# Optimization experiments

Measured on AMD Instinct MI355X. Metric: run time of the kernel, lower is better.

The kernel has to match this reference:

```python
import jax, jax.numpy as jnp
import numpy as np

B, H, W, C = 8, 64, 64, 512
CK, CV = C // 8, C // 2  # 64, 256


def maxpool2x2(x):
    # x: [B, H, W, C] -> [B, H//2, W//2, C], 2x2 max pool, stride 2 (keras MaxPooling2D default)
    b, h, w, c = x.shape
    return x.reshape(b, h // 2, 2, w // 2, 2, c).max(axis=(2, 4))


def setup_inputs() -> dict:
    key = jax.random.key(0)
    ks = jax.random.split(key, 6)
    wscale = 0.02
    return {
        "x": jax.random.normal(ks[0], (B, H, W, C), dtype=jnp.float32),
        "w_theta": jax.random.normal(ks[1], (C, CK), dtype=jnp.float32) * wscale,
        "w_phi": jax.random.normal(ks[2], (C, CK), dtype=jnp.float32) * wscale,
        "w_g": jax.random.normal(ks[3], (C, CV), dtype=jnp.float32) * wscale,
        "w_o": jax.random.normal(ks[4], (CV, C), dtype=jnp.float32) * wscale,
        "gamma": jax.random.normal(ks[5], (1,), dtype=jnp.float32),
    }


def reference(x, w_theta, w_phi, w_g, w_o, gamma):
    b, h, w, c = x.shape
    hw = h * w
    # theta: 1x1 conv -> [B, HW, C//8]
    theta = jnp.einsum('bhwc,ck->bhwk', x, w_theta).reshape(b, hw, -1)
    # phi: 1x1 conv + 2x2 maxpool -> [B, HW//4, C//8]
    phi = maxpool2x2(jnp.einsum('bhwc,ck->bhwk', x, w_phi)).reshape(b, hw // 4, -1)
    # attention: [B, HW, HW//4], softmax over last axis
    attn = jax.nn.softmax(jnp.einsum('bqk,bpk->bqp', theta, phi), axis=-1)
    # g: 1x1 conv + 2x2 maxpool -> [B, HW//4, C//2]
    g = maxpool2x2(jnp.einsum('bhwc,cv->bhwv', x, w_g)).reshape(b, hw // 4, -1)
    # attn_g: [B, HW, C//2] -> [B, H, W, C//2] -> 1x1 conv -> [B, H, W, C]
    attn_g = jnp.einsum('bqp,bpv->bqv', attn, g).reshape(b, h, w, -1)
    attn_g = jnp.einsum('bhwv,vc->bhwc', attn_g, w_o)
    return x + gamma * attn_g
```

## Files before the change

kernel.cpp:

```cpp
#include <hip/hip_runtime.h>
#include <hip/hip_bf16.h>
#include <cstddef>
#include <cstdint>


typedef __attribute__((ext_vector_type(8))) short short8;
typedef __attribute__((ext_vector_type(4))) float float4v;

namespace {
constexpr int kB = 8, kC = 512, kCK = 64, kCV = 256, kHW = 4096, kP = 1024;
constexpr int kNP = 384;
}

__device__ __forceinline__ void gll16(const void* g, void* l) {
  __builtin_amdgcn_global_load_lds((uint32_t __attribute__((address_space(1)))*)g,
                                   (uint32_t __attribute__((address_space(3)))*)l,
                                   16, 0, 0);
}
__device__ __forceinline__ float4v mfma16(short8 a, short8 b, float4v c) {
  return __builtin_amdgcn_mfma_f32_16x16x32_bf16(a, b, c, 0, 0, 0);
}
__device__ __forceinline__ const short8* fragp(const char* tile, int row, int oct) {
  return (const short8*)(tile + row * 128 + ((oct ^ (row & 7)) * 16));
}

__global__ __launch_bounds__(256) void k_pack_w(
    const float* __restrict__ wt, const float* __restrict__ wphi,
    const float* __restrict__ wg, const float* __restrict__ wo,
    __hip_bfloat16* __restrict__ wAll, __hip_bfloat16* __restrict__ woT) {
  int idx = blockIdx.x * 256 + threadIdx.x;
  if (idx < 196608) {
    int n = idx >> 9, k = idx & 511;
    float v = (n < 64) ? wt[k * 64 + n]
            : (n < 128) ? wphi[k * 64 + (n - 64)]
                        : wg[k * 256 + (n - 128)];
    wAll[idx] = __float2bfloat16(v);
  } else {
    int t = idx - 196608;
    int n = t >> 8, k = t & 255;
    woT[t] = __float2bfloat16(wo[k * 512 + n]);
  }
}

__global__ __launch_bounds__(256) void k_proj(const float* __restrict__ x,
                                              const __hip_bfloat16* __restrict__ wAll,
                                              __hip_bfloat16* __restrict__ pgf) {
  __shared__ __align__(16) char smem[16384 + 49152];
  char* As = smem;
  char* Bs = smem + 16384;
  const int tid = threadIdx.x, wid = tid >> 6, lane = tid & 63;
  const int m = lane & 15, quad = lane >> 4;
  const int row0 = blockIdx.x * 64;
  const int wm = (wid >> 1) * 32, wn = (wid & 1) * 192;
  float4v acc[2][12] = {};
  for (int kc = 0; kc < 512; kc += 64) {
#pragma unroll
    for (int u = 0; u < 4; ++u) {
      const int r0 = (wid * 4 + u) * 4;
      const int row = r0 + (lane >> 4);
      const int sqg = (lane & 15) ^ (row & 15);
      gll16(x + (size_t)(row0 + row) * 512 + kc + sqg * 4, As + r0 * 256);
    }
#pragma unroll
    for (int u = 0; u < 12; ++u) {
      const int r0 = (wid * 12 + u) * 8;
      const int row = r0 + (lane >> 3);
      const int og = (lane & 7) ^ (row & 7);
      gll16(wAll + (size_t)row * 512 + kc + og * 8, Bs + r0 * 128);
    }
    __syncthreads();
#pragma unroll
    for (int kk = 0; kk < 64; kk += 32) {
      short8 af[2];
#pragma unroll
      for (int i = 0; i < 2; ++i) {
        const int row = wm + i * 16 + m;
        const int sq0 = (kk >> 2) + quad * 2;
        float4v lo = *(const float4v*)(As + row * 256 + ((sq0 ^ m) * 16));
        float4v hi = *(const float4v*)(As + row * 256 + (((sq0 + 1) ^ m) * 16));
        short8 a;
        a[0] = __builtin_bit_cast(short, __float2bfloat16(lo[0]));
        a[1] = __builtin_bit_cast(short, __float2bfloat16(lo[1]));
        a[2] = __builtin_bit_cast(short, __float2bfloat16(lo[2]));
        a[3] = __builtin_bit_cast(short, __float2bfloat16(lo[3]));
        a[4] = __builtin_bit_cast(short, __float2bfloat16(hi[0]));
        a[5] = __builtin_bit_cast(short, __float2bfloat16(hi[1]));
        a[6] = __builtin_bit_cast(short, __float2bfloat16(hi[2]));
        a[7] = __builtin_bit_cast(short, __float2bfloat16(hi[3]));
        af[i] = a;
      }
      const int oct = (kk >> 3) + quad;
#pragma unroll
      for (int j = 0; j < 12; ++j) {
        short8 bf = *fragp(Bs, wn + j * 16 + m, oct);
#pragma unroll
        for (int i = 0; i < 2; ++i) acc[i][j] = mfma16(af[i], bf, acc[i][j]);
      }
    }
    __syncthreads();
  }
#pragma unroll
  for (int i = 0; i < 2; ++i)
#pragma unroll
    for (int j = 0; j < 12; ++j)
#pragma unroll
      for (int r = 0; r < 4; ++r)
        pgf[(size_t)(row0 + wm + i * 16 + quad * 4 + r) * 384 + wn + j * 16 + m] =
            __float2bfloat16(acc[i][j][r]);
}

__global__ __launch_bounds__(256) void k_pool_phi(const __hip_bfloat16* __restrict__ pg,
                                                  __hip_bfloat16* __restrict__ phi_p) {
  int idx = blockIdx.x * 256 + threadIdx.x;
  int c = idx & 63;
  int p = (idx >> 6) & 1023;
  int b = idx >> 16;
  int ph = p >> 5, pw = p & 31;
  size_t base = ((size_t)b * 4096 + ph * 128 + pw * 2) * kNP + 64 + c;
  float v0 = __bfloat162float(pg[base]);
  float v1 = __bfloat162float(pg[base + kNP]);
  float v2 = __bfloat162float(pg[base + kNP * 64]);
  float v3 = __bfloat162float(pg[base + kNP * 64 + kNP]);
  phi_p[idx] = __float2bfloat16(fmaxf(fmaxf(v0, v1), fmaxf(v2, v3)));
}

__global__ __launch_bounds__(256) void k_pool_gT(const __hip_bfloat16* __restrict__ pg,
                                                 __hip_bfloat16* __restrict__ gT) {
  __shared__ __hip_bfloat16 t[64][65];
  const int p0 = blockIdx.x * 64, v0 = blockIdx.y * 64, b = blockIdx.z;
#pragma unroll
  for (int it = 0; it < 16; ++it) {
    int li = it * 256 + threadIdx.x;
    int pp = li >> 6, v = li & 63;
    int p = p0 + pp;
    int ph = p >> 5, pw = p & 31;
    size_t base = ((size_t)b * 4096 + ph * 128 + pw * 2) * kNP + 128 + v0 + v;
    float mv = fmaxf(
        fmaxf(__bfloat162float(pg[base]), __bfloat162float(pg[base + kNP])),
        fmaxf(__bfloat162float(pg[base + kNP * 64]), __bfloat162float(pg[base + kNP * 64 + kNP])));
    t[pp][v] = __float2bfloat16(mv);
  }
  __syncthreads();
#pragma unroll
  for (int it = 0; it < 16; ++it) {
    int li = it * 256 + threadIdx.x;
    int v = li >> 6, p = li & 63;
    gT[((size_t)b * 256 + v0 + v) * 1024 + p0 + p] = t[p][v];
  }
}

__global__ __launch_bounds__(1024) void k_fattn(
    const __hip_bfloat16* __restrict__ pgf,
    const __hip_bfloat16* __restrict__ phip,
    const __hip_bfloat16* __restrict__ gT,
    __hip_bfloat16* __restrict__ O) {
  __shared__ __align__(16) char smem[131072 + 2048 + 256];
  char* P = smem;
  float* pred = (float*)(smem + 131072);
  float* rowstat = (float*)(smem + 131072 + 2048);

  const int tid = threadIdx.x, wid = tid >> 6, lane = tid & 63;
  const int m = lane & 15, quad = lane >> 4;
  const int bid = blockIdx.x;
  const int b = bid & 7;
  const int q0 = (bid >> 3) * 64;
  const int qh = wid & 1;
  const int kw = wid >> 1;

  short8 aq[2][2];
  const __hip_bfloat16* qb = pgf + (size_t)(b * kHW + q0 + qh * 32) * kNP;
#pragma unroll
  for (int i = 0; i < 2; ++i)
#pragma unroll
    for (int t = 0; t < 2; ++t)
      aq[i][t] = *(const short8*)(qb + (size_t)(i * 16 + m) * kNP + t * 32 + quad * 8);

  const __hip_bfloat16* kbp = phip + ((size_t)b * kP + kw * 128) * 64;
  float4v sc[2][8] = {};
  short8 kf[2][2];
#pragma unroll
  for (int t = 0; t < 2; ++t)
    kf[0][t] = *(const short8*)(kbp + (size_t)m * 64 + t * 32 + quad * 8);
#pragma unroll
  for (int c = 0; c < 8; ++c) {
    if (c < 7) {
#pragma unroll
      for (int t = 0; t < 2; ++t)
        kf[(c + 1) & 1][t] =
            *(const short8*)(kbp + (size_t)((c + 1) * 16 + m) * 64 + t * 32 + quad * 8);
    }
#pragma unroll
    for (int t = 0; t < 2; ++t)
#pragma unroll
      for (int i = 0; i < 2; ++i) sc[i][c] = mfma16(aq[i][t], kf[c & 1][t], sc[i][c]);
  }

  float mx[2][4];
#pragma unroll
  for (int i = 0; i < 2; ++i)
#pragma unroll
    for (int r = 0; r < 4; ++r) {
      float v = sc[i][0][r];
#pragma unroll
      for (int s = 1; s < 8; ++s) v = fmaxf(v, sc[i][s][r]);
#pragma unroll
      for (int d = 1; d < 16; d <<= 1) v = fmaxf(v, __shfl_xor(v, d));
      mx[i][r] = v;
    }
  if (m == 0) {
#pragma unroll
    for (int i = 0; i < 2; ++i)
#pragma unroll
      for (int r = 0; r < 4; ++r)
        pred[(qh * 32 + i * 16 + quad * 4 + r) * 8 + kw] = mx[i][r];
  }
  __syncthreads();
  if (tid < 64) {
    float v = pred[tid * 8];
#pragma unroll
    for (int w = 1; w < 8; ++w) v = fmaxf(v, pred[tid * 8 + w]);
    rowstat[tid] = v;
  }
  __syncthreads();
  float sm[2][4];
#pragma unroll
  for (int i = 0; i < 2; ++i)
#pragma unroll
    for (int r = 0; r < 4; ++r) {
      const float rm = rowstat[qh * 32 + i * 16 + quad * 4 + r];
      float s = 0.f;
#pragma unroll
      for (int ss = 0; ss < 8; ++ss) {
        float e = __expf(sc[i][ss][r] - rm);
        sc[i][ss][r] = e;
        s += e;
      }
#pragma unroll
      for (int d = 1; d < 16; d <<= 1) s += __shfl_xor(s, d);
      sm[i][r] = s;
    }
  if (m == 0) {
#pragma unroll
    for (int i = 0; i < 2; ++i)
#pragma unroll
      for (int r = 0; r < 4; ++r)
        pred[(qh * 32 + i * 16 + quad * 4 + r) * 8 + kw] = sm[i][r];
  }
  __syncthreads();
  if (tid < 64) {
    float s = 0.f;
#pragma unroll
    for (int w = 0; w < 8; ++w) s += pred[tid * 8 + w];
    rowstat[tid] = 1.f / s;
  }
  __syncthreads();

#pragma unroll
  for (int i = 0; i < 2; ++i)
#pragma unroll
    for (int c = 0; c < 8; ++c)
#pragma unroll
      for (int r = 0; r < 4; ++r) {
        const int row = qh * 32 + i * 16 + quad * 4 + r;
        const int key = kw * 128 + c * 16 + m;
        const int oct = key >> 3;
        const int oc2 = (oct & 0x70) | ((oct & 15) ^ (row & 15));
        *(__hip_bfloat16*)(P + row * 2048 + oc2 * 16 + (key & 7) * 2) =
            __float2bfloat16(sc[i][c][r]);
      }
  __syncthreads();

  const __hip_bfloat16* gbase = gT + ((size_t)b * kCV + wid * 16 + m) * kP;
  float4v oc[4] = {};
  short8 gf[2];
  gf[0] = *(const short8*)(gbase + quad * 8);
#pragma unroll
  for (int cp = 0; cp < 32; ++cp) {
    const int cur = cp & 1;
    if (cp < 31) gf[cur ^ 1] = *(const short8*)(gbase + (cp + 1) * 32 + quad * 8);
    short8 af[4];
#pragma unroll
    for (int i = 0; i < 4; ++i) {
      const int row = i * 16 + m;
      const int oct = cp * 4 + quad;
      const int oc2 = (oct & 0x70) | ((oct & 15) ^ (row & 15));
      af[i] = *(const short8*)(P + row * 2048 + oc2 * 16);
    }
#pragma unroll
    for (int i = 0; i < 4; ++i) oc[i] = mfma16(af[i], gf[cur], oc[i]);
  }

#pragma unroll
  for (int i = 0; i < 4; ++i)
#pragma unroll
    for (int r = 0; r < 4; ++r) {
      const int row = i * 16 + quad * 4 + r;
      O[((size_t)b * kHW + q0 + row) * kCV + wid * 16 + m] =
          __float2bfloat16(oc[i][r] * rowstat[row]);
    }
}

__global__ __launch_bounds__(256) void k_out(const __hip_bfloat16* __restrict__ A,
                                             const __hip_bfloat16* __restrict__ Bw,
                                             const float* __restrict__ x,
                                             const float* __restrict__ gamma,
                                             float* __restrict__ out) {
  __shared__ __align__(16) char smem[4 * 16384];
  const int tid = threadIdx.x, wid = tid >> 6, lane = tid & 63;
  const int m = lane & 15, quad = lane >> 4;
  const int row0 = blockIdx.x * 128, col0 = blockIdx.y * 128;
  const int wm = (wid >> 1) * 64, wn = (wid & 1) * 64;
  float4v acc[4][4] = {};
  auto stage = [&](int t, int buf) {
    const int kc = t * 64;
#pragma unroll
    for (int u = 0; u < 4; ++u) {
      const int r0 = (wid * 4 + u) * 8;
      const int row = r0 + (lane >> 3);
      const int og = (lane & 7) ^ (row & 7);
      gll16(A + (size_t)(row0 + row) * 256 + kc + og * 8, smem + buf * 16384 + r0 * 128);
      gll16(Bw + (size_t)(col0 + row) * 256 + kc + og * 8,
            smem + 32768 + buf * 16384 + r0 * 128);
    }
  };
  stage(0, 0);
  __syncthreads();
#pragma unroll
  for (int t = 0; t < 4; ++t) {
    if (t < 3) stage(t + 1, (t + 1) & 1);
    const char* Ab = smem + (t & 1) * 16384;
    const char* Bb = smem + 32768 + (t & 1) * 16384;
    __builtin_amdgcn_s_setprio(1);
#pragma unroll
    for (int kk = 0; kk < 64; kk += 32) {
      const int oct = (kk >> 3) + quad;
      short8 af[4], bf[4];
#pragma unroll
      for (int i = 0; i < 4; ++i) af[i] = *fragp(Ab, wm + i * 16 + m, oct);
#pragma unroll
      for (int j = 0; j < 4; ++j) bf[j] = *fragp(Bb, wn + j * 16 + m, oct);
#pragma unroll
      for (int i = 0; i < 4; ++i)
#pragma unroll
        for (int j = 0; j < 4; ++j) acc[i][j] = mfma16(af[i], bf[j], acc[i][j]);
    }
    __builtin_amdgcn_s_setprio(0);
    __syncthreads();
  }
  const float g = gamma[0];
#pragma unroll
  for (int i = 0; i < 4; ++i)
#pragma unroll
    for (int j = 0; j < 4; ++j) {
      const int cc = col0 + wn + j * 16 + m;
      const int rb = row0 + wm + i * 16 + quad * 4;
#pragma unroll
      for (int r = 0; r < 4; ++r) {
        const size_t idx = (size_t)(rb + r) * 512 + cc;
        out[idx] = x[idx] + g * acc[i][j][r];
      }
    }
}

extern "C" void kernel_launch(void* const* d_in, const int* in_sizes, int n_in,
                              void* d_out, int out_size, void* d_ws, size_t ws_size,
                              hipStream_t stream) {
  (void)in_sizes; (void)n_in; (void)out_size; (void)ws_size;
  const float* x     = (const float*)d_in[0];
  const float* wt    = (const float*)d_in[1];
  const float* wphi  = (const float*)d_in[2];
  const float* wg    = (const float*)d_in[3];
  const float* wo    = (const float*)d_in[4];
  const float* gamma = (const float*)d_in[5];
  float* out = (float*)d_out;

  char* ws = (char*)d_ws;
  __hip_bfloat16* wAll = (__hip_bfloat16*)(ws);
  __hip_bfloat16* woT  = (__hip_bfloat16*)(ws + 393216);
  __hip_bfloat16* pgf  = (__hip_bfloat16*)(ws + 655360);
  __hip_bfloat16* phip = (__hip_bfloat16*)(ws + 25821184);
  __hip_bfloat16* gT   = (__hip_bfloat16*)(ws + 26869760);
  __hip_bfloat16* O    = (__hip_bfloat16*)(ws + 31064064);

  k_pack_w<<<1280, 256, 0, stream>>>(wt, wphi, wg, wo, wAll, woT);
  k_proj<<<512, 256, 0, stream>>>(x, wAll, pgf);
  k_pool_phi<<<2048, 256, 0, stream>>>(pgf, phip);
  k_pool_gT<<<dim3(16, 4, 8), 256, 0, stream>>>(pgf, gT);
  k_fattn<<<dim3(kHW / 64 * kB), 1024, 0, stream>>>(pgf, phip, gT, O);
  k_out<<<dim3(256, 4), 256, 0, stream>>>(O, woT, x, gamma, out);
}
```

Before: 234.9 us.

## Repartition attention waves over all query rows and split PV across key halves

Each of the 16 waves in the fused attention kernel now computes all 64 query rows against a 64-key slice, where before each wave handled 32 rows against 128 keys. This reuses the query fragments and deepens key prefetch to three buffers. The PV stage now gives each wave a 64x32 output tile over half of the keys, reusing A and G fragments more and prefetching deeper. A shared-memory reduction then combines the two key-halves. One barrier before the P write is dropped, the reduction adds LDS traffic and two barriers, and the higher register pressure is capped by a launch_bounds hint.

```diff
diff --git a/kernel.cpp b/kernel.cpp
--- a/kernel.cpp
+++ b/kernel.cpp
@@ -149,120 +149,104 @@
   }
 }
 
-__global__ __launch_bounds__(1024) void k_fattn(
+__global__ __launch_bounds__(1024, 4) void k_fattn(
     const __hip_bfloat16* __restrict__ pgf,
     const __hip_bfloat16* __restrict__ phip,
     const __hip_bfloat16* __restrict__ gT,
     __hip_bfloat16* __restrict__ O) {
-  __shared__ __align__(16) char smem[131072 + 2048 + 256];
+  __shared__ __align__(16) char smem[131072 + 4096 + 256];
   char* P = smem;
   float* pred = (float*)(smem + 131072);
-  float* rowstat = (float*)(smem + 131072 + 2048);
+  float* rowstat = (float*)(smem + 131072 + 4096);
 
   const int tid = threadIdx.x, wid = tid >> 6, lane = tid & 63;
   const int m = lane & 15, quad = lane >> 4;
   const int bid = blockIdx.x;
   const int b = bid & 7;
   const int q0 = (bid >> 3) * 64;
-  const int qh = wid & 1;
-  const int kw = wid >> 1;
-
-  short8 aq[2][2];
-  const __hip_bfloat16* qb = pgf + (size_t)(b * kHW + q0 + qh * 32) * kNP;
-#pragma unroll
-  for (int i = 0; i < 2; ++i)
+
+  short8 aq[4][2];
+  const __hip_bfloat16* qb = pgf + (size_t)(b * kHW + q0) * kNP;
+#pragma unroll
+  for (int i = 0; i < 4; ++i)
 #pragma unroll
     for (int t = 0; t < 2; ++t)
       aq[i][t] = *(const short8*)(qb + (size_t)(i * 16 + m) * kNP + t * 32 + quad * 8);
 
-  const __hip_bfloat16* kbp = phip + ((size_t)b * kP + kw * 128) * 64;
-  float4v sc[2][8] = {};
-  short8 kf[2][2];
-#pragma unroll
-  for (int t = 0; t < 2; ++t)
+  const __hip_bfloat16* kbp = phip + ((size_t)b * kP + wid * 64) * 64;
+  float4v sc[4][4] = {};
+  short8 kf[3][2];
+#pragma unroll
+  for (int t = 0; t < 2; ++t) {
     kf[0][t] = *(const short8*)(kbp + (size_t)m * 64 + t * 32 + quad * 8);
-#pragma unroll
-  for (int c = 0; c < 8; ++c) {
-    if (c < 7) {
+    kf[1][t] = *(const short8*)(kbp + (size_t)(16 + m) * 64 + t * 32 + quad * 8);
+  }
+#pragma unroll
+  for (int c = 0; c < 4; ++c) {
+    if (c < 2) {
 #pragma unroll
       for (int t = 0; t < 2; ++t)
-        kf[(c + 1) & 1][t] =
-            *(const short8*)(kbp + (size_t)((c + 1) * 16 + m) * 64 + t * 32 + quad * 8);
+        kf[(c + 2) % 3][t] =
+            *(const short8*)(kbp + (size_t)((c + 2) * 16 + m) * 64 + t * 32 + quad * 8);
     }
 #pragma unroll
     for (int t = 0; t < 2; ++t)
 #pragma unroll
-      for (int i = 0; i < 2; ++i) sc[i][c] = mfma16(aq[i][t], kf[c & 1][t], sc[i][c]);
-  }
-
-  float mx[2][4];
-#pragma unroll
-  for (int i = 0; i < 2; ++i)
+      for (int i = 0; i < 4; ++i) sc[i][c] = mfma16(aq[i][t], kf[c % 3][t], sc[i][c]);
+  }
+
+#pragma unroll
+  for (int i = 0; i < 4; ++i) {
 #pragma unroll
     for (int r = 0; r < 4; ++r) {
       float v = sc[i][0][r];
 #pragma unroll
-      for (int s = 1; s < 8; ++s) v = fmaxf(v, sc[i][s][r]);
+      for (int c = 1; c < 4; ++c) v = fmaxf(v, sc[i][c][r]);
 #pragma unroll
       for (int d = 1; d < 16; d <<= 1) v = fmaxf(v, __shfl_xor(v, d));
-      mx[i][r] = v;
-    }
-  if (m == 0) {
-#pragma unroll
-    for (int i = 0; i < 2; ++i)
-#pragma unroll
-      for (int r = 0; r < 4; ++r)
-        pred[(qh * 32 + i * 16 + quad * 4 + r) * 8 + kw] = mx[i][r];
+      if (m == 0) pred[(i * 16 + quad * 4 + r) * 16 + wid] = v;
+    }
   }
   __syncthreads();
   if (tid < 64) {
-    float v = pred[tid * 8];
-#pragma unroll
-    for (int w = 1; w < 8; ++w) v = fmaxf(v, pred[tid * 8 + w]);
+    float v = pred[tid * 16];
+#pragma unroll
+    for (int w = 1; w < 16; ++w) v = fmaxf(v, pred[tid * 16 + w]);
     rowstat[tid] = v;
   }
   __syncthreads();
-  float sm[2][4];
-#pragma unroll
-  for (int i = 0; i < 2; ++i)
+#pragma unroll
+  for (int i = 0; i < 4; ++i)
 #pragma unroll
     for (int r = 0; r < 4; ++r) {
-      const float rm = rowstat[qh * 32 + i * 16 + quad * 4 + r];
+      const float rm = rowstat[i * 16 + quad * 4 + r];
       float s = 0.f;
 #pragma unroll
-      for (int ss = 0; ss < 8; ++ss) {
-        float e = __expf(sc[i][ss][r] - rm);
-        sc[i][ss][r] = e;
+      for (int c = 0; c < 4; ++c) {
+        float e = __expf(sc[i][c][r] - rm);
+        sc[i][c][r] = e;
         s += e;
       }
 #pragma unroll
       for (int d = 1; d < 16; d <<= 1) s += __shfl_xor(s, d);
-      sm[i][r] = s;
-    }
-  if (m == 0) {
-#pragma unroll
-    for (int i = 0; i < 2; ++i)
-#pragma unroll
-      for (int r = 0; r < 4; ++r)
-        pred[(qh * 32 + i * 16 + quad * 4 + r) * 8 + kw] = sm[i][r];
-  }
+      if (m == 0) pred[(i * 16 + quad * 4 + r) * 16 + wid] = s;
+    }
   __syncthreads();
   if (tid < 64) {
     float s = 0.f;
 #pragma unroll
-    for (int w = 0; w < 8; ++w) s += pred[tid * 8 + w];
+    for (int w = 0; w < 16; ++w) s += pred[tid * 16 + w];
     rowstat[tid] = 1.f / s;
   }
-  __syncthreads();
-
-#pragma unroll
-  for (int i = 0; i < 2; ++i)
-#pragma unroll
-    for (int c = 0; c < 8; ++c)
+
+#pragma unroll
+  for (int i = 0; i < 4; ++i)
+#pragma unroll
+    for (int c = 0; c < 4; ++c)
 #pragma unroll
       for (int r = 0; r < 4; ++r) {
-        const int row = qh * 32 + i * 16 + quad * 4 + r;
-        const int key = kw * 128 + c * 16 + m;
+        const int row = i * 16 + quad * 4 + r;
+        const int key = wid * 64 + c * 16 + m;
         const int oct = key >> 3;
         const int oc2 = (oct & 0x70) | ((oct & 15) ^ (row & 15));
         *(__hip_bfloat16*)(P + row * 2048 + oc2 * 16 + (key & 7) * 2) =
@@ -270,34 +254,70 @@
       }
   __syncthreads();
 
-  const __hip_bfloat16* gbase = gT + ((size_t)b * kCV + wid * 16 + m) * kP;
-  float4v oc[4] = {};
-  short8 gf[2];
-  gf[0] = *(const short8*)(gbase + quad * 8);
-#pragma unroll
-  for (int cp = 0; cp < 32; ++cp) {
-    const int cur = cp & 1;
-    if (cp < 31) gf[cur ^ 1] = *(const short8*)(gbase + (cp + 1) * 32 + quad * 8);
-    short8 af[4];
-#pragma unroll
-    for (int i = 0; i < 4; ++i) {
-      const int row = i * 16 + m;
-      const int oct = cp * 4 + quad;
-      const int oc2 = (oct & 0x70) | ((oct & 15) ^ (row & 15));
-      af[i] = *(const short8*)(P + row * 2048 + oc2 * 16);
-    }
-#pragma unroll
-    for (int i = 0; i < 4; ++i) oc[i] = mfma16(af[i], gf[cur], oc[i]);
-  }
-
-#pragma unroll
-  for (int i = 0; i < 4; ++i)
-#pragma unroll
-    for (int r = 0; r < 4; ++r) {
-      const int row = i * 16 + quad * 4 + r;
-      O[((size_t)b * kHW + q0 + row) * kCV + wid * 16 + m] =
-          __float2bfloat16(oc[i][r] * rowstat[row]);
-    }
+  const int g = wid >> 3, w8 = wid & 7;
+  const __hip_bfloat16* gb = gT + ((size_t)b * kCV + w8 * 32) * kP + g * 512;
+  float4v oc[4][2] = {};
+  short8 gf[3][2], af[2][4];
+  auto ldG = [&](int cp, int j) {
+    return *(const short8*)(gb + (size_t)(j * 16 + m) * kP + cp * 32 + quad * 8);
+  };
+  auto ldA = [&](int cp, int i) {
+    const int row = i * 16 + m;
+    const int oct = (g * 16 + cp) * 4 + quad;
+    const int oc2 = (oct & 0x70) | ((oct & 15) ^ (row & 15));
+    return *(const short8*)(P + row * 2048 + oc2 * 16);
+  };
+#pragma unroll
+  for (int j = 0; j < 2; ++j) {
+    gf[0][j] = ldG(0, j);
+    gf[1][j] = ldG(1, j);
+  }
+#pragma unroll
+  for (int i = 0; i < 4; ++i) af[0][i] = ldA(0, i);
+#pragma unroll
+  for (int cp = 0; cp < 16; ++cp) {
+    if (cp < 15) {
+#pragma unroll
+      for (int i = 0; i < 4; ++i) af[(cp + 1) & 1][i] = ldA(cp + 1, i);
+    }
+    if (cp < 14) {
+#pragma unroll
+      for (int j = 0; j < 2; ++j) gf[(cp + 2) % 3][j] = ldG(cp + 2, j);
+    }
+#pragma unroll
+    for (int i = 0; i < 4; ++i)
+#pragma unroll
+      for (int j = 0; j < 2; ++j)
+        oc[i][j] = mfma16(af[cp & 1][i], gf[cp % 3][j], oc[i][j]);
+  }
+
+  __syncthreads();
+  float* Pf = (float*)smem;
+  if (g == 1) {
+#pragma unroll
+    for (int i = 0; i < 4; ++i)
+#pragma unroll
+      for (int j = 0; j < 2; ++j)
+#pragma unroll
+        for (int r = 0; r < 4; ++r) {
+          const int row = i * 16 + quad * 4 + r;
+          Pf[row * 260 + w8 * 32 + j * 16 + m] = oc[i][j][r];
+        }
+  }
+  __syncthreads();
+  if (g == 0) {
+#pragma unroll
+    for (int i = 0; i < 4; ++i)
+#pragma unroll
+      for (int j = 0; j < 2; ++j)
+#pragma unroll
+        for (int r = 0; r < 4; ++r) {
+          const int row = i * 16 + quad * 4 + r;
+          const int col = w8 * 32 + j * 16 + m;
+          const float s = (oc[i][j][r] + Pf[row * 260 + col]) * rowstat[row];
+          O[((size_t)b * kHW + q0 + row) * kCV + col] = __float2bfloat16(s);
+        }
+  }
 }
 
 __global__ __launch_bounds__(256) void k_out(const __hip_bfloat16* __restrict__ A,
```

New measurement: 241.4 us. 1.03x slower.

## Rewrite attention as single-wave online-softmax flash kernel with register-resident P

Applied to the files above, without the earlier changes.

Replaces the 1024-thread block attention kernel, which kept the full 64x1024 probability tile in LDS and used block-wide syncs for the softmax statistics. The new kernel runs one wave per block. Each block handles 32 queries and 128 value channels and streams keys in chunks of 64 with an online softmax. Probabilities are repacked from the QK accumulator layout into the PV input-fragment layout using cross-lane shuffles, so LDS and barriers are not needed. The cost is recomputing QK^T once per value group (twice overall), plus heavy register pressure and many uncoalesced per-lane global loads of K and G with no LDS staging.

```diff
diff --git a/kernel.cpp b/kernel.cpp
--- a/kernel.cpp
+++ b/kernel.cpp
@@ -6,6 +6,7 @@
 
 typedef __attribute__((ext_vector_type(8))) short short8;
 typedef __attribute__((ext_vector_type(4))) float float4v;
+typedef __attribute__((ext_vector_type(4))) uint32_t uint4v;
 
 namespace {
 constexpr int kB = 8, kC = 512, kCK = 64, kCV = 256, kHW = 4096, kP = 1024;
@@ -22,6 +23,17 @@
 }
 __device__ __forceinline__ const short8* fragp(const char* tile, int row, int oct) {
   return (const short8*)(tile + row * 128 + ((oct ^ (row & 7)) * 16));
+}
+__device__ __forceinline__ uint32_t packbf(float a, float b) {
+  const uint32_t lo = (uint32_t)__builtin_bit_cast(unsigned short, __float2bfloat16(a));
+  const uint32_t hi = (uint32_t)__builtin_bit_cast(unsigned short, __float2bfloat16(b));
+  return lo | (hi << 16);
+}
+__device__ __forceinline__ uint32_t sx16(uint32_t v) {
+  return (uint32_t)__shfl_xor((int)v, 16);
+}
+__device__ __forceinline__ uint32_t sx32(uint32_t v) {
+  return (uint32_t)__shfl_xor((int)v, 32);
 }
 
 __global__ __launch_bounds__(256) void k_pack_w(
@@ -149,155 +161,148 @@
   }
 }
 
-__global__ __launch_bounds__(1024) void k_fattn(
+__global__ __launch_bounds__(64, 2) void k_fattn(
     const __hip_bfloat16* __restrict__ pgf,
     const __hip_bfloat16* __restrict__ phip,
     const __hip_bfloat16* __restrict__ gT,
     __hip_bfloat16* __restrict__ O) {
-  __shared__ __align__(16) char smem[131072 + 2048 + 256];
-  char* P = smem;
-  float* pred = (float*)(smem + 131072);
-  float* rowstat = (float*)(smem + 131072 + 2048);
-
-  const int tid = threadIdx.x, wid = tid >> 6, lane = tid & 63;
+  const int lane = threadIdx.x;
   const int m = lane & 15, quad = lane >> 4;
   const int bid = blockIdx.x;
   const int b = bid & 7;
-  const int q0 = (bid >> 3) * 64;
-  const int qh = wid & 1;
-  const int kw = wid >> 1;
-
-  short8 aq[2][2];
-  const __hip_bfloat16* qb = pgf + (size_t)(b * kHW + q0 + qh * 32) * kNP;
-#pragma unroll
-  for (int i = 0; i < 2; ++i)
-#pragma unroll
-    for (int t = 0; t < 2; ++t)
-      aq[i][t] = *(const short8*)(qb + (size_t)(i * 16 + m) * kNP + t * 32 + quad * 8);
-
-  const __hip_bfloat16* kbp = phip + ((size_t)b * kP + kw * 128) * 64;
-  float4v sc[2][8] = {};
-  short8 kf[2][2];
-#pragma unroll
-  for (int t = 0; t < 2; ++t)
-    kf[0][t] = *(const short8*)(kbp + (size_t)m * 64 + t * 32 + quad * 8);
-#pragma unroll
-  for (int c = 0; c < 8; ++c) {
-    if (c < 7) {
-#pragma unroll
-      for (int t = 0; t < 2; ++t)
-        kf[(c + 1) & 1][t] =
-            *(const short8*)(kbp + (size_t)((c + 1) * 16 + m) * 64 + t * 32 + quad * 8);
-    }
-#pragma unroll
-    for (int t = 0; t < 2; ++t)
-#pragma unroll
-      for (int i = 0; i < 2; ++i) sc[i][c] = mfma16(aq[i][t], kf[c & 1][t], sc[i][c]);
-  }
-
-  float mx[2][4];
-#pragma unroll
-  for (int i = 0; i < 2; ++i)
-#pragma unroll
-    for (int r = 0; r < 4; ++r) {
-      float v = sc[i][0][r];
-#pragma unroll
-      for (int s = 1; s < 8; ++s) v = fmaxf(v, sc[i][s][r]);
-#pragma unroll
-      for (int d = 1; d < 16; d <<= 1) v = fmaxf(v, __shfl_xor(v, d));
-      mx[i][r] = v;
-    }
-  if (m == 0) {
-#pragma unroll
-    for (int i = 0; i < 2; ++i)
-#pragma unroll
-      for (int r = 0; r < 4; ++r)
-        pred[(qh * 32 + i * 16 + quad * 4 + r) * 8 + kw] = mx[i][r];
-  }
-  __syncthreads();
-  if (tid < 64) {
-    float v = pred[tid * 8];
-#pragma unroll
-    for (int w = 1; w < 8; ++w) v = fmaxf(v, pred[tid * 8 + w]);
-    rowstat[tid] = v;
-  }
-  __syncthreads();
-  float sm[2][4];
-#pragma unroll
-  for (int i = 0; i < 2; ++i)
-#pragma unroll
-    for (int r = 0; r < 4; ++r) {
-      const float rm = rowstat[qh * 32 + i * 16 + quad * 4 + r];
-      float s = 0.f;
-#pragma unroll
-      for (int ss = 0; ss < 8; ++ss) {
-        float e = __expf(sc[i][ss][r] - rm);
-        sc[i][ss][r] = e;
-        s += e;
-      }
-#pragma unroll
-      for (int d = 1; d < 16; d <<= 1) s += __shfl_xor(s, d);
-      sm[i][r] = s;
-    }
-  if (m == 0) {
-#pragma unroll
-    for (int i = 0; i < 2; ++i)
-#pragma unroll
-      for (int r = 0; r < 4; ++r)
-        pred[(qh * 32 + i * 16 + quad * 4 + r) * 8 + kw] = sm[i][r];
-  }
-  __syncthreads();
-  if (tid < 64) {
-    float s = 0.f;
-#pragma unroll
-    for (int w = 0; w < 8; ++w) s += pred[tid * 8 + w];
-    rowstat[tid] = 1.f / s;
-  }
-  __syncthreads();
-
-#pragma unroll
-  for (int i = 0; i < 2; ++i)
-#pragma unroll
-    for (int c = 0; c < 8; ++c)
+  const int rest = bid >> 3;
+  const int q0 = (rest & 127) * 32;
+  const int vg = rest >> 7;
+
+  const __hip_bfloat16* qbase = pgf + (size_t)(b * kHW + q0) * kNP;
+  const __hip_bfloat16* kbase = phip + (size_t)b * kP * 64;
+  const __hip_bfloat16* gbase = gT + ((size_t)b * kCV + vg * 128) * kP;
+
+  short8 qf[2][2];
+#pragma unroll
+  for (int qt = 0; qt < 2; ++qt)
+#pragma unroll
+    for (int chh = 0; chh < 2; ++chh)
+      qf[qt][chh] =
+          *(const short8*)(qbase + (size_t)(qt * 16 + m) * kNP + chh * 32 + quad * 8);
+
+  float4v oc[2][8] = {};
+  float mrun[2] = {-3e38f, -3e38f};
+  float lrun[2] = {0.f, 0.f};
+
+  short8 kf[4][2];
+#pragma unroll
+  for (int kt = 0; kt < 4; ++kt)
+#pragma unroll
+    for (int chh = 0; chh < 2; ++chh)
+      kf[kt][chh] =
+          *(const short8*)(kbase + (size_t)(kt * 16 + m) * 64 + chh * 32 + quad * 8);
+
+  for (int c = 0; c < 16; ++c) {
+    short8 g0[8];
+#pragma unroll
+    for (int vt = 0; vt < 8; ++vt)
+      g0[vt] = *(const short8*)(gbase + (size_t)(vt * 16 + m) * kP + c * 64 + quad * 8);
+
+    float4v sct[2][4] = {};
+#pragma unroll
+    for (int kt = 0; kt < 4; ++kt)
+#pragma unroll
+      for (int chh = 0; chh < 2; ++chh)
+#pragma unroll
+        for (int qt = 0; qt < 2; ++qt)
+          sct[qt][kt] = mfma16(kf[kt][chh], qf[qt][chh], sct[qt][kt]);
+
+    if (c < 15) {
+#pragma unroll
+      for (int kt = 0; kt < 4; ++kt)
+#pragma unroll
+        for (int chh = 0; chh < 2; ++chh)
+          kf[kt][chh] = *(const short8*)(kbase +
+              (size_t)((c + 1) * 64 + kt * 16 + m) * 64 + chh * 32 + quad * 8);
+    }
+    short8 g1[8];
+#pragma unroll
+    for (int vt = 0; vt < 8; ++vt)
+      g1[vt] =
+          *(const short8*)(gbase + (size_t)(vt * 16 + m) * kP + c * 64 + 32 + quad * 8);
+
+#pragma unroll
+    for (int qt = 0; qt < 2; ++qt) {
+      float cmax = sct[qt][0][0];
+#pragma unroll
+      for (int kt = 0; kt < 4; ++kt)
+#pragma unroll
+        for (int r = 0; r < 4; ++r) cmax = fmaxf(cmax, sct[qt][kt][r]);
+      cmax = fmaxf(cmax, __shfl_xor(cmax, 16));
+      cmax = fmaxf(cmax, __shfl_xor(cmax, 32));
+      const float mnew = fmaxf(mrun[qt], cmax);
+      const float corr = __expf(mrun[qt] - mnew);
+      mrun[qt] = mnew;
+      float psum = 0.f;
+#pragma unroll
+      for (int kt = 0; kt < 4; ++kt)
+#pragma unroll
+        for (int r = 0; r < 4; ++r) {
+          const float e = __expf(sct[qt][kt][r] - mnew);
+          sct[qt][kt][r] = e;
+          psum += e;
+        }
+      psum += __shfl_xor(psum, 16);
+      psum += __shfl_xor(psum, 32);
+      lrun[qt] = lrun[qt] * corr + psum;
+      float corr_r[4];
+#pragma unroll
+      for (int r = 0; r < 4; ++r) corr_r[r] = __shfl(corr, quad * 4 + r, 16);
+#pragma unroll
+      for (int vt = 0; vt < 8; ++vt)
+#pragma unroll
+        for (int r = 0; r < 4; ++r) oc[qt][vt][r] *= corr_r[r];
+
+#pragma unroll
+      for (int t = 0; t < 2; ++t) {
+        const uint32_t X0 = packbf(sct[qt][2 * t][0], sct[qt][2 * t][1]);
+        const uint32_t X1 = packbf(sct[qt][2 * t][2], sct[qt][2 * t][3]);
+        const uint32_t Y0 = packbf(sct[qt][2 * t + 1][0], sct[qt][2 * t + 1][1]);
+        const uint32_t Y1 = packbf(sct[qt][2 * t + 1][2], sct[qt][2 * t + 1][3]);
+        const uint32_t X0p = sx16(X0), X1p = sx16(X1), Y0p = sx16(Y0), Y1p = sx16(Y1);
+        const bool odd = (quad & 1) != 0;
+        const uint32_t Xe0 = odd ? X0p : X0, Xe1 = odd ? X1p : X1;
+        const uint32_t Xo0 = odd ? X0 : X0p, Xo1 = odd ? X1 : X1p;
+        const uint32_t Ye0 = odd ? Y0p : Y0, Ye1 = odd ? Y1p : Y1;
+        const uint32_t Yo0 = odd ? Y0 : Y0p, Yo1 = odd ? Y1 : Y1p;
+        const uint32_t Xe0h = sx32(Xe0), Xe1h = sx32(Xe1);
+        const uint32_t Xo0h = sx32(Xo0), Xo1h = sx32(Xo1);
+        const uint32_t Ye0h = sx32(Ye0), Ye1h = sx32(Ye1);
+        const uint32_t Yo0h = sx32(Yo0), Yo1h = sx32(Yo1);
+        uint4v dv;
+        dv[0] = quad == 0 ? Xe0 : quad == 1 ? Xe0h : quad == 2 ? Ye0h : Ye0;
+        dv[1] = quad == 0 ? Xe1 : quad == 1 ? Xe1h : quad == 2 ? Ye1h : Ye1;
+        dv[2] = quad == 0 ? Xo0 : quad == 1 ? Xo0h : quad == 2 ? Yo0h : Yo0;
+        dv[3] = quad == 0 ? Xo1 : quad == 1 ? Xo1h : quad == 2 ? Yo1h : Yo1;
+        const short8 af = __builtin_bit_cast(short8, dv);
+#pragma unroll
+        for (int vt = 0; vt < 8; ++vt)
+          oc[qt][vt] = mfma16(af, (t == 0 ? g0[vt] : g1[vt]), oc[qt][vt]);
+      }
+    }
+  }
+
+#pragma unroll
+  for (int qt = 0; qt < 2; ++qt) {
+    const float inv = 1.f / lrun[qt];
+    float inv_r[4];
+#pragma unroll
+    for (int r = 0; r < 4; ++r) inv_r[r] = __shfl(inv, quad * 4 + r, 16);
+#pragma unroll
+    for (int vt = 0; vt < 8; ++vt)
 #pragma unroll
       for (int r = 0; r < 4; ++r) {
-        const int row = qh * 32 + i * 16 + quad * 4 + r;
-        const int key = kw * 128 + c * 16 + m;
-        const int oct = key >> 3;
-        const int oc2 = (oct & 0x70) | ((oct & 15) ^ (row & 15));
-        *(__hip_bfloat16*)(P + row * 2048 + oc2 * 16 + (key & 7) * 2) =
-            __float2bfloat16(sc[i][c][r]);
-      }
-  __syncthreads();
-
-  const __hip_bfloat16* gbase = gT + ((size_t)b * kCV + wid * 16 + m) * kP;
-  float4v oc[4] = {};
-  short8 gf[2];
-  gf[0] = *(const short8*)(gbase + quad * 8);
-#pragma unroll
-  for (int cp = 0; cp < 32; ++cp) {
-    const int cur = cp & 1;
-    if (cp < 31) gf[cur ^ 1] = *(const short8*)(gbase + (cp + 1) * 32 + quad * 8);
-    short8 af[4];
-#pragma unroll
-    for (int i = 0; i < 4; ++i) {
-      const int row = i * 16 + m;
-      const int oct = cp * 4 + quad;
-      const int oc2 = (oct & 0x70) | ((oct & 15) ^ (row & 15));
-      af[i] = *(const short8*)(P + row * 2048 + oc2 * 16);
-    }
-#pragma unroll
-    for (int i = 0; i < 4; ++i) oc[i] = mfma16(af[i], gf[cur], oc[i]);
-  }
-
-#pragma unroll
-  for (int i = 0; i < 4; ++i)
-#pragma unroll
-    for (int r = 0; r < 4; ++r) {
-      const int row = i * 16 + quad * 4 + r;
-      O[((size_t)b * kHW + q0 + row) * kCV + wid * 16 + m] =
-          __float2bfloat16(oc[i][r] * rowstat[row]);
-    }
+        const int row = q0 + qt * 16 + quad * 4 + r;
+        O[((size_t)b * kHW + row) * kCV + vg * 128 + vt * 16 + m] =
+            __float2bfloat16(oc[qt][vt][r] * inv_r[r]);
+      }
+  }
 }
 
 __global__ __launch_bounds__(256) void k_out(const __hip_bfloat16* __restrict__ A,
@@ -386,6 +391,6 @@
   k_proj<<<512, 256, 0, stream>>>(x, wAll, pgf);
   k_pool_phi<<<2048, 256, 0, stream>>>(pgf, phip);
   k_pool_gT<<<dim3(16, 4, 8), 256, 0, stream>>>(pgf, gT);
-  k_fattn<<<dim3(kHW / 64 * kB), 1024, 0, stream>>>(pgf, phip, gT, O);
+  k_fattn<<<dim3(2048), 64, 0, stream>>>(pgf, phip, gT, O);
   k_out<<<dim3(256, 4), 256, 0, stream>>>(O, woT, x, gamma, out);
 }
```

Result: slower. 265.5 us (+13.0%).
